# Kernel optimization log

Hardware: AMD Instinct MI355X
Metric: run time of the kernel (lower is better)

Reference implementation:

```python
import jax, jax.numpy as jnp
import numpy as np

N_POINTS = 100000
K_VOL = 27          # 3^3 hypercube kernel offsets
PAIRS = 60000       # active in/out pairs per kernel offset
C_IN = 64
C_OUT = 64


def setup_inputs() -> dict:
    key = jax.random.key(0)
    k1, k2, k3, k4, k5 = jax.random.split(key, 5)
    stdv = 1.0 / np.sqrt(C_IN * K_VOL)  # matches reset_parameters
    inputs = {
        "input": jax.random.normal(k1, (N_POINTS, C_IN), dtype=jnp.float32),
        "kernel": jax.random.uniform(k2, (K_VOL, C_IN, C_OUT), dtype=jnp.float32,
                                      minval=-stdv, maxval=stdv),
        "bias": jax.random.uniform(k3, (1, C_OUT), dtype=jnp.float32,
                                    minval=-stdv, maxval=stdv),
        # per-offset kernel maps (normally produced from coordinate hashing in metadata)
        "in_map": jax.random.randint(k4, (K_VOL, PAIRS), 0, N_POINTS, dtype=jnp.int32),
        "out_map": jax.random.randint(k5, (K_VOL, PAIRS), 0, N_POINTS, dtype=jnp.int32),
    }
    return inputs


def reference(input, kernel, bias, in_map, out_map):
    # Sparse convolution: for each kernel offset k, gather input rows via
    # in_map[k], apply the per-offset GEMM with kernel[k], and scatter-add
    # the results into the output rows given by out_map[k].
    K, P = in_map.shape
    n_out = input.shape[0]
    gathered = input[in_map]                         # [K, P, Cin]  (gather)
    per_offset = jnp.einsum('kpi,kio->kpo', gathered, kernel)  # [K, P, Cout] (GEMM)
    out = jax.ops.segment_sum(per_offset.reshape(K * P, -1),
                              out_map.reshape(-1),
                              num_segments=n_out)    # [N, Cout] (scatter-add)
    return out + bias
```

## Files before the change

### kernel.cpp

```cpp
#include <hip/hip_runtime.h>
#include <hip/hip_bf16.h>

#define N_POINTS 100000
#define K_VOL 27
#define PAIRS 60000
#define CCH 64
#define TILES_PER_K (PAIRS / 16)
#define BX 64
#define NWAVES 4

#define RPB 64
#define NBUCKETS ((N_POINTS + RPB - 1) / RPB)
#define NBINS (NBUCKETS * K_VOL)
#define CAP 96
#define SENT 0xFFFFFFFFu
#define CNTSTRIDE 32

#define PREP_BLKS 6250
#define FILL_BLKS (K_VOL * 64)
#define PSUB (PAIRS / 8)
#define NLB 200

#define WS_ENT 0
#define WS_CNT (NBINS * CAP * 4)
#define WS_INBF (WS_CNT + NBUCKETS * CNTSTRIDE * 4)
#define WS_WT (WS_INBF + N_POINTS * CCH * 2)
#define WS_NEED (WS_WT + K_VOL * CCH * CCH * 2)

typedef __bf16 bf16x8 __attribute__((ext_vector_type(8)));
typedef __bf16 bf16x4 __attribute__((ext_vector_type(4)));
typedef float f32x4 __attribute__((ext_vector_type(4)));


__global__ __launch_bounds__(256) void prep_fill_kernel(
    const float* __restrict__ input, const float* __restrict__ weight,
    const int* __restrict__ in_map, const int* __restrict__ out_map,
    unsigned char* __restrict__ ws) {
  const int bid = blockIdx.x;
  if (bid < PREP_BLKS) {
    int t = bid * 256 + threadIdx.x;
    float4 v = ((const float4*)input)[t];
    bf16x4 o;
    o[0] = (__bf16)v.x; o[1] = (__bf16)v.y; o[2] = (__bf16)v.z; o[3] = (__bf16)v.w;
    *(bf16x4*)(ws + WS_INBF + (size_t)t * 8) = o;
    if (t < K_VOL * CCH * CCH) {
      int k = t >> 12;
      int r = t & 4095;
      int ci = r >> 6, co = r & 63;
      *(__bf16*)(ws + WS_WT + (size_t)(((k * 64 + co) << 6) + ci) * 2) =
          (__bf16)weight[t];
    }
  } else {
    __shared__ unsigned int lcnt[NLB];
    __shared__ unsigned int lcur[NLB];
    const int f = bid - PREP_BLKS;
    const int k = f >> 6;
    const int bx = f & 63;
    const int slice = bx & 7;
    const int sub = bx >> 3;
    const int pbeg = sub * PSUB, pend = pbeg + PSUB;
    const int* omp_ = out_map + k * PAIRS;
    const int* imp_ = in_map + k * PAIRS;
    unsigned int* cntp = (unsigned int*)(ws + WS_CNT);
    unsigned int* entp = (unsigned int*)(ws + WS_ENT);

    for (int i = threadIdx.x; i < NLB; i += 256) lcnt[i] = 0;
    __syncthreads();

    for (int p = pbeg + (int)threadIdx.x * 4; p < pend; p += 1024) {
      int4 om4 = *(const int4*)(omp_ + p);
      int oms[4] = {om4.x, om4.y, om4.z, om4.w};
#pragma unroll
      for (int j = 0; j < 4; ++j) {
        int bkt = oms[j] >> 6;
        if ((bkt & 7) == slice) atomicAdd(&lcnt[bkt >> 3], 1u);
      }
    }
    __syncthreads();

    for (int lb = threadIdx.x; lb < NLB; lb += 256) {
      unsigned n = lcnt[lb];
      if (n) {
        int bkt = (lb << 3) | slice;
        lcur[lb] = atomicAdd(cntp + (bkt << 5) + k, n);
      }
    }
    __syncthreads();

    for (int p = pbeg + (int)threadIdx.x * 4; p < pend; p += 1024) {
      int4 om4 = *(const int4*)(omp_ + p);
      int4 im4 = *(const int4*)(imp_ + p);
      int oms[4] = {om4.x, om4.y, om4.z, om4.w};
      int ims[4] = {im4.x, im4.y, im4.z, im4.w};
#pragma unroll
      for (int j = 0; j < 4; ++j) {
        int bkt = oms[j] >> 6;
        if ((bkt & 7) != slice) continue;
        unsigned pos = atomicAdd(&lcur[bkt >> 3], 1u);
        if (pos < CAP)
          entp[(bkt * K_VOL + k) * CAP + pos] =
              (unsigned)ims[j] | ((unsigned)(oms[j] & 63) << 17);
      }
    }
  }
}

__global__ __launch_bounds__(256) void spconv_main_kernel(
    const float* __restrict__ bias, const unsigned char* __restrict__ ws,
    float* __restrict__ out) {
  __shared__ __align__(16) unsigned char lds[4 * 8192];
  const unsigned int* cnt = (const unsigned int*)(ws + WS_CNT);
  const unsigned int* entries = (const unsigned int*)(ws + WS_ENT);
  const __bf16* inbf = (const __bf16*)(ws + WS_INBF);
  const __bf16* wt = (const __bf16*)(ws + WS_WT);

  const int b = blockIdx.x;
  const int tid = threadIdx.x;
  const int wave = tid >> 6, lane = tid & 63;
  const int c = lane & 15, q = lane >> 4;
  unsigned char* stage = lds + wave * 8192;
  unsigned char* pmat = stage + 4096;

#pragma unroll
  for (int i = 0; i < 16; ++i)
    *(float*)(pmat + i * 256 + lane * 4) = 0.f;

  f32x4 acc[4][4];
#pragma unroll
  for (int rb = 0; rb < 4; ++rb)
#pragma unroll
    for (int nt = 0; nt < 4; ++nt) acc[rb][nt] = (f32x4){0.f, 0.f, 0.f, 0.f};

  bf16x8 bfA0[4], bfA1[4];

  auto grow = [&](unsigned v, bf16x8& x0, bf16x8& x1) {
    unsigned r = (v == SENT) ? 0u : (v & 0x1FFFFu);
    const __bf16* ar = inbf + ((size_t)r << 6);
    x0 = *(const bf16x8*)(ar + q * 8);
    x1 = *(const bf16x8*)(ar + 32 + q * 8);
  };

  auto do_tile = [&](unsigned entL, unsigned entH, bf16x8 aL0, bf16x8 aL1,
                     bf16x8 aH0, bf16x8 aH1) {
    int mol0 = -1, mol1 = -1;
    if (q == 0 && entL != SENT) mol0 = (int)(entL >> 17);
    if (q == 1 && entH != SENT) mol1 = (int)(entH >> 17);
    if (mol0 >= 0) {
      int m = c;
      *(__bf16*)(pmat + mol0 * 64 + (((m >> 3) ^ (mol0 & 3)) << 4) + (m & 7) * 2) =
          (__bf16)1.0f;
    }
    if (mol1 >= 0) {
      int m = 16 + c;
      *(__bf16*)(pmat + mol1 * 64 + (((m >> 3) ^ (mol1 & 3)) << 4) + (m & 7) * 2) =
          (__bf16)1.0f;
    }

    f32x4 c1a[4], c1b[4];
#pragma unroll
    for (int nt = 0; nt < 4; ++nt) {
      c1a[nt] = (f32x4){0.f, 0.f, 0.f, 0.f};
      c1b[nt] = (f32x4){0.f, 0.f, 0.f, 0.f};
    }
#pragma unroll
    for (int nt = 0; nt < 4; ++nt) {
      c1a[nt] = __builtin_amdgcn_mfma_f32_16x16x32_bf16(aL0, bfA0[nt], c1a[nt],
                                                        0, 0, 0);
      c1a[nt] = __builtin_amdgcn_mfma_f32_16x16x32_bf16(aL1, bfA1[nt], c1a[nt],
                                                        0, 0, 0);
      c1b[nt] = __builtin_amdgcn_mfma_f32_16x16x32_bf16(aH0, bfA0[nt], c1b[nt],
                                                        0, 0, 0);
      c1b[nt] = __builtin_amdgcn_mfma_f32_16x16x32_bf16(aH1, bfA1[nt], c1b[nt],
                                                        0, 0, 0);
    }

#pragma unroll
    for (int nt = 0; nt < 4; ++nt) {
      const int n = nt * 16 + c;
      const int swz = n & 3;
      const int in0 = (q & 1) * 8;
      bf16x4 h0, h1;
#pragma unroll
      for (int r = 0; r < 4; ++r) {
        h0[r] = (__bf16)c1a[nt][r];
        h1[r] = (__bf16)c1b[nt][r];
      }
      *(bf16x4*)(stage + n * 64 + (((q >> 1) ^ swz) << 4) + in0) = h0;
      *(bf16x4*)(stage + n * 64 + (((2 + (q >> 1)) ^ swz) << 4) + in0) = h1;
    }

    bf16x8 pfrag[4];
#pragma unroll
    for (int rb = 0; rb < 4; ++rb)
      pfrag[rb] = *(const bf16x8*)(pmat + (rb * 16 + c) * 64 + ((q ^ (c & 3)) << 4));
#pragma unroll
    for (int nt = 0; nt < 4; ++nt) {
      const int n = nt * 16 + c;
      const bf16x8 bb = *(const bf16x8*)(stage + n * 64 + ((q ^ (n & 3)) << 4));
#pragma unroll
      for (int rb = 0; rb < 4; ++rb)
        acc[rb][nt] = __builtin_amdgcn_mfma_f32_16x16x32_bf16(pfrag[rb], bb,
                                                             acc[rb][nt], 0, 0, 0);
    }

    if (mol0 >= 0) {
      int m = c;
      *(__bf16*)(pmat + mol0 * 64 + (((m >> 3) ^ (mol0 & 3)) << 4) + (m & 7) * 2) =
          (__bf16)0.0f;
    }
    if (mol1 >= 0) {
      int m = 16 + c;
      *(__bf16*)(pmat + mol1 * 64 + (((m >> 3) ^ (mol1 & 3)) << 4) + (m & 7) * 2) =
          (__bf16)0.0f;
    }
  };

  int j = wave;
  unsigned ec, w0, w1, w2, w3;
  bf16x8 qa00, qa01, qa10, qa11, qa20, qa21, qa30, qa31;
  unsigned ecn, x0, x1, x2, x3;
  {
    unsigned cn0 = cnt[(b << 5) + j];
    const unsigned* bp0 = entries + (size_t)(b * K_VOL + j) * CAP;
    unsigned a0 = bp0[c], a1 = bp0[16 + c], a2 = bp0[32 + c], a3 = bp0[48 + c];
    unsigned cn1 = 0, b0 = SENT, b1 = SENT, b2 = SENT, b3 = SENT;
    if (j + 4 < K_VOL) {
      cn1 = cnt[(b << 5) + j + 4];
      const unsigned* bp1 = entries + (size_t)(b * K_VOL + j + 4) * CAP;
      b0 = bp1[c]; b1 = bp1[16 + c]; b2 = bp1[32 + c]; b3 = bp1[48 + c];
    }
    ec = cn0 > CAP ? (unsigned)CAP : cn0;
    w0 = ((unsigned)c < ec) ? a0 : SENT;
    w1 = ((unsigned)(16 + c) < ec) ? a1 : SENT;
    w2 = ((unsigned)(32 + c) < ec) ? a2 : SENT;
    w3 = ((unsigned)(48 + c) < ec) ? a3 : SENT;
    grow(w0, qa00, qa01); grow(w1, qa10, qa11);
    grow(w2, qa20, qa21); grow(w3, qa30, qa31);
    ecn = cn1 > CAP ? (unsigned)CAP : cn1;
    x0 = ((unsigned)c < ecn) ? b0 : SENT;
    x1 = ((unsigned)(16 + c) < ecn) ? b1 : SENT;
    x2 = ((unsigned)(32 + c) < ecn) ? b2 : SENT;
    x3 = ((unsigned)(48 + c) < ecn) ? b3 : SENT;
  }
#pragma unroll
  for (int nt = 0; nt < 4; ++nt) {
    const __bf16* wrow = wt + ((j * 64 + nt * 16 + c) << 6);
    bfA0[nt] = *(const bf16x8*)(wrow + q * 8);
    bfA1[nt] = *(const bf16x8*)(wrow + 32 + q * 8);
  }

  while (j < K_VOL) {
    const int jn = j + 4, jf = j + 8;
    const bool hasn = jn < K_VOL, hasf = jf < K_VOL;

    bf16x8 pa00, pa01, pa10, pa11, pa20, pa21, pa30, pa31;
    if (hasn) {
      grow(x0, pa00, pa01); grow(x1, pa10, pa11);
      grow(x2, pa20, pa21); grow(x3, pa30, pa31);
    }

    unsigned fc = 0, h0 = SENT, h1 = SENT, h2 = SENT, h3 = SENT;
    if (hasf) {
      fc = cnt[(b << 5) + jf];
      const unsigned* bpf = entries + (size_t)(b * K_VOL + jf) * CAP;
      h0 = bpf[c]; h1 = bpf[16 + c]; h2 = bpf[32 + c]; h3 = bpf[48 + c];
    }

    if (ec) do_tile(w0, w1, qa00, qa01, qa10, qa11);
    if (ec > 32) do_tile(w2, w3, qa20, qa21, qa30, qa31);
    for (unsigned tb = 64; tb < ec; tb += 32) {
      const unsigned* base = entries + (size_t)(b * K_VOL + j) * CAP;
      unsigned i0 = tb + c, i1 = tb + 16 + c;
      unsigned e0 = (i0 < ec) ? base[i0] : SENT;
      unsigned e1 = (i1 < ec) ? base[i1] : SENT;
      bf16x8 y00, y01, y10, y11;
      grow(e0, y00, y01);
      grow(e1, y10, y11);
      do_tile(e0, e1, y00, y01, y10, y11);
    }

    if (hasn) {
#pragma unroll
      for (int nt = 0; nt < 4; ++nt) {
        const __bf16* wrow = wt + ((jn * 64 + nt * 16 + c) << 6);
        bfA0[nt] = *(const bf16x8*)(wrow + q * 8);
        bfA1[nt] = *(const bf16x8*)(wrow + 32 + q * 8);
      }
    }

    ec = ecn;
    w0 = x0; w1 = x1; w2 = x2; w3 = x3;
    qa00 = pa00; qa01 = pa01; qa10 = pa10; qa11 = pa11;
    qa20 = pa20; qa21 = pa21; qa30 = pa30; qa31 = pa31;
    ecn = fc > CAP ? (unsigned)CAP : fc;
    x0 = ((unsigned)c < ecn) ? h0 : SENT;
    x1 = ((unsigned)(16 + c) < ecn) ? h1 : SENT;
    x2 = ((unsigned)(32 + c) < ecn) ? h2 : SENT;
    x3 = ((unsigned)(48 + c) < ecn) ? h3 : SENT;
    j = jn;
  }

  __syncthreads();
  float* bufA = (float*)lds;
  float* bufB = (float*)(lds + 16384);

  auto REDST = [&](float* buf) {
#pragma unroll
    for (int rb = 0; rb < 4; ++rb)
#pragma unroll
      for (int nt = 0; nt < 4; ++nt)
#pragma unroll
        for (int r = 0; r < 4; ++r) {
          int row = rb * 16 + q * 4 + r;
          int col = (nt * 16 + c) ^ (q << 2) ^ ((q & 1) << 4);
          buf[row * 64 + col] = acc[rb][nt][r];
        }
  };
  auto REDADD = [&](const float* buf) {
#pragma unroll
    for (int rb = 0; rb < 4; ++rb)
#pragma unroll
      for (int nt = 0; nt < 4; ++nt)
#pragma unroll
        for (int r = 0; r < 4; ++r) {
          int row = rb * 16 + q * 4 + r;
          int col = (nt * 16 + c) ^ (q << 2) ^ ((q & 1) << 4);
          acc[rb][nt][r] += buf[row * 64 + col];
        }
  };

  if (wave == 1) REDST(bufA);
  if (wave == 3) REDST(bufB);
  __syncthreads();
  if (wave == 0) REDADD(bufA);
  if (wave == 2) REDADD(bufB);
  __syncthreads();
  if (wave == 2) REDST(bufA);
  __syncthreads();
  if (wave == 0) {
    REDADD(bufA);
    float bv[4];
#pragma unroll
    for (int nt = 0; nt < 4; ++nt) bv[nt] = bias[nt * 16 + c];
#pragma unroll
    for (int rb = 0; rb < 4; ++rb)
#pragma unroll
      for (int r = 0; r < 4; ++r) {
        const int row = b * RPB + rb * 16 + q * 4 + r;
        if (row < N_POINTS) {
#pragma unroll
          for (int nt = 0; nt < 4; ++nt)
            out[row * CCH + nt * 16 + c] = acc[rb][nt][r] + bv[nt];
        }
      }
  }
}


__global__ __launch_bounds__(256) void init_out_kernel(
    const float* __restrict__ bias, float* __restrict__ out) {
  int tid = blockIdx.x * blockDim.x + threadIdx.x;
  int c4 = tid & 15;
  float4 b = ((const float4*)bias)[c4];
  ((float4*)out)[tid] = b;
}

__global__ __launch_bounds__(256) void spconv_kernel(
    const float* __restrict__ input, const float* __restrict__ weight,
    const int* __restrict__ in_map, const int* __restrict__ out_map,
    float* __restrict__ out) {
  const int k = blockIdx.y;
  const int lane = threadIdx.x & 63;
  const int wave = threadIdx.x >> 6;
  const int col = lane & 15;
  const int quad = lane >> 4;

  const float* Wk = weight + k * (CCH * CCH);
  bf16x8 bfrag[4][2];
#pragma unroll
  for (int nt = 0; nt < 4; ++nt) {
    int co = nt * 16 + col;
#pragma unroll
    for (int s = 0; s < 2; ++s) {
      int ci0 = s * 32 + quad * 8;
      bf16x8 f;
#pragma unroll
      for (int j = 0; j < 8; ++j) f[j] = (__bf16)Wk[(ci0 + j) * CCH + co];
      bfrag[nt][s] = f;
    }
  }

  const int* im = in_map + k * PAIRS;
  const int* om = out_map + k * PAIRS;

  for (int tile = blockIdx.x * NWAVES + wave; tile < TILES_PER_K;
       tile += BX * NWAVES) {
    const int pbase = tile * 16;
    int rin = im[pbase + col];
    const float* arow = input + rin * CCH;
    bf16x8 afrag[2];
#pragma unroll
    for (int s = 0; s < 2; ++s) {
      const float4 x0 = *(const float4*)(arow + s * 32 + quad * 8);
      const float4 x1 = *(const float4*)(arow + s * 32 + quad * 8 + 4);
      bf16x8 f;
      f[0] = (__bf16)x0.x; f[1] = (__bf16)x0.y;
      f[2] = (__bf16)x0.z; f[3] = (__bf16)x0.w;
      f[4] = (__bf16)x1.x; f[5] = (__bf16)x1.y;
      f[6] = (__bf16)x1.z; f[7] = (__bf16)x1.w;
      afrag[s] = f;
    }

    f32x4 acc[4];
#pragma unroll
    for (int nt = 0; nt < 4; ++nt) acc[nt] = (f32x4){0.f, 0.f, 0.f, 0.f};
#pragma unroll
    for (int nt = 0; nt < 4; ++nt) {
      acc[nt] = __builtin_amdgcn_mfma_f32_16x16x32_bf16(afrag[0], bfrag[nt][0],
                                                        acc[nt], 0, 0, 0);
      acc[nt] = __builtin_amdgcn_mfma_f32_16x16x32_bf16(afrag[1], bfrag[nt][1],
                                                        acc[nt], 0, 0, 0);
    }

    int orow[4];
#pragma unroll
    for (int r = 0; r < 4; ++r) orow[r] = om[pbase + quad * 4 + r];
#pragma unroll
    for (int r = 0; r < 4; ++r) {
      float* op = out + orow[r] * CCH + col;
#pragma unroll
      for (int nt = 0; nt < 4; ++nt) atomicAdd(op + nt * 16, acc[nt][r]);
    }
  }
}


extern "C" void kernel_launch(void* const* d_in, const int* in_sizes, int n_in,
                              void* d_out, int out_size, void* d_ws,
                              size_t ws_size, hipStream_t stream) {
  const float* input = (const float*)d_in[0];
  const float* weight = (const float*)d_in[1];
  const float* bias = (const float*)d_in[2];
  const int* in_map = (const int*)d_in[3];
  const int* out_map = (const int*)d_in[4];
  float* out = (float*)d_out;

  if (d_ws != nullptr && ws_size >= (size_t)WS_NEED) {
    unsigned char* ws = (unsigned char*)d_ws;
    hipMemsetAsync(ws + WS_CNT, 0, NBUCKETS * CNTSTRIDE * 4, stream);
    prep_fill_kernel<<<PREP_BLKS + FILL_BLKS, 256, 0, stream>>>(
        input, weight, in_map, out_map, ws);
    spconv_main_kernel<<<NBUCKETS, 256, 0, stream>>>(bias, ws, out);
  } else {
    init_out_kernel<<<(N_POINTS * 16) / 256, 256, 0, stream>>>(bias, out);
    dim3 grid(BX, K_VOL);
    spconv_kernel<<<grid, 256, 0, stream>>>(input, weight, in_map, out_map, out);
  }
}
```

Baseline: 227.2 us.

## Buffer bucket entries in LDS during fill and change LDS swizzle pattern

The fill phase now reads in_map and out_map only once. It stages each pair's packed entry in a per-bucket LDS buffer, with an overflow path that appends directly to global memory via atomics. The buffered entries are then copied out per bucket after the global offset is reserved. This removes the second pass over the maps and the scattered global writes. Separately, the XOR swizzle for the pmat and stage LDS tiles now keys on (row>>1)&3 instead of row&3, to reduce LDS bank conflicts for the 8-byte and 16-byte accesses. The overflow path could reorder entries and adds atomic contention, and the larger shared buffer raises LDS use per fill block.

```diff
diff --git a/kernel.cpp b/kernel.cpp
--- a/kernel.cpp
+++ b/kernel.cpp
@@ -20,6 +20,7 @@
 #define FILL_BLKS (K_VOL * 64)
 #define PSUB (PAIRS / 8)
 #define NLB 200
+#define CAPL 24
 
 #define WS_ENT 0
 #define WS_CNT (NBINS * CAP * 4)
@@ -53,6 +54,7 @@
   } else {
     __shared__ unsigned int lcnt[NLB];
     __shared__ unsigned int lcur[NLB];
+    __shared__ unsigned int lbuf[NLB * CAPL];
     const int f = bid - PREP_BLKS;
     const int k = f >> 6;
     const int bx = f & 63;
@@ -69,11 +71,23 @@
 
     for (int p = pbeg + (int)threadIdx.x * 4; p < pend; p += 1024) {
       int4 om4 = *(const int4*)(omp_ + p);
+      int4 im4 = *(const int4*)(imp_ + p);
       int oms[4] = {om4.x, om4.y, om4.z, om4.w};
+      int ims[4] = {im4.x, im4.y, im4.z, im4.w};
 #pragma unroll
       for (int j = 0; j < 4; ++j) {
         int bkt = oms[j] >> 6;
-        if ((bkt & 7) == slice) atomicAdd(&lcnt[bkt >> 3], 1u);
+        if ((bkt & 7) != slice) continue;
+        int lb = bkt >> 3;
+        unsigned ent = (unsigned)ims[j] | ((unsigned)(oms[j] & 63) << 17);
+        unsigned pos = atomicAdd(&lcnt[lb], 1u);
+        if (pos < CAPL) {
+          lbuf[lb * CAPL + pos] = ent;
+        } else {
+          atomicSub(&lcnt[lb], 1u);
+          unsigned gp = atomicAdd(cntp + (bkt << 5) + k, 1u);
+          if (gp < CAP) entp[(size_t)(bkt * K_VOL + k) * CAP + gp] = ent;
+        }
       }
     }
     __syncthreads();
@@ -87,19 +101,15 @@
     }
     __syncthreads();
 
-    for (int p = pbeg + (int)threadIdx.x * 4; p < pend; p += 1024) {
-      int4 om4 = *(const int4*)(omp_ + p);
-      int4 im4 = *(const int4*)(imp_ + p);
-      int oms[4] = {om4.x, om4.y, om4.z, om4.w};
-      int ims[4] = {im4.x, im4.y, im4.z, im4.w};
-#pragma unroll
-      for (int j = 0; j < 4; ++j) {
-        int bkt = oms[j] >> 6;
-        if ((bkt & 7) != slice) continue;
-        unsigned pos = atomicAdd(&lcur[bkt >> 3], 1u);
-        if (pos < CAP)
-          entp[(bkt * K_VOL + k) * CAP + pos] =
-              (unsigned)ims[j] | ((unsigned)(oms[j] & 63) << 17);
+    for (int lb = threadIdx.x; lb < NLB; lb += 256) {
+      unsigned n = lcnt[lb];
+      if (!n) continue;
+      int bkt = (lb << 3) | slice;
+      unsigned base = lcur[lb];
+      unsigned int* dst = entp + (size_t)(bkt * K_VOL + k) * CAP;
+      for (unsigned i = 0; i < n; ++i) {
+        unsigned pos = base + i;
+        if (pos < CAP) dst[pos] = lbuf[lb * CAPL + i];
       }
     }
   }
@@ -147,13 +157,13 @@
     if (q == 1 && entH != SENT) mol1 = (int)(entH >> 17);
     if (mol0 >= 0) {
       int m = c;
-      *(__bf16*)(pmat + mol0 * 64 + (((m >> 3) ^ (mol0 & 3)) << 4) + (m & 7) * 2) =
-          (__bf16)1.0f;
+      *(__bf16*)(pmat + mol0 * 64 + (((m >> 3) ^ ((mol0 >> 1) & 3)) << 4) +
+                 (m & 7) * 2) = (__bf16)1.0f;
     }
     if (mol1 >= 0) {
       int m = 16 + c;
-      *(__bf16*)(pmat + mol1 * 64 + (((m >> 3) ^ (mol1 & 3)) << 4) + (m & 7) * 2) =
-          (__bf16)1.0f;
+      *(__bf16*)(pmat + mol1 * 64 + (((m >> 3) ^ ((mol1 >> 1) & 3)) << 4) +
+                 (m & 7) * 2) = (__bf16)1.0f;
     }
 
     f32x4 c1a[4], c1b[4];
@@ -177,7 +187,7 @@
 #pragma unroll
     for (int nt = 0; nt < 4; ++nt) {
       const int n = nt * 16 + c;
-      const int swz = n & 3;
+      const int swz = (n >> 1) & 3;
       const int in0 = (q & 1) * 8;
       bf16x4 h0, h1;
 #pragma unroll
@@ -192,11 +202,13 @@
     bf16x8 pfrag[4];
 #pragma unroll
     for (int rb = 0; rb < 4; ++rb)
-      pfrag[rb] = *(const bf16x8*)(pmat + (rb * 16 + c) * 64 + ((q ^ (c & 3)) << 4));
+      pfrag[rb] = *(const bf16x8*)(pmat + (rb * 16 + c) * 64 +
+                                   ((q ^ ((c >> 1) & 3)) << 4));
 #pragma unroll
     for (int nt = 0; nt < 4; ++nt) {
       const int n = nt * 16 + c;
-      const bf16x8 bb = *(const bf16x8*)(stage + n * 64 + ((q ^ (n & 3)) << 4));
+      const bf16x8 bb = *(const bf16x8*)(stage + n * 64 +
+                                         ((q ^ ((n >> 1) & 3)) << 4));
 #pragma unroll
       for (int rb = 0; rb < 4; ++rb)
         acc[rb][nt] = __builtin_amdgcn_mfma_f32_16x16x32_bf16(pfrag[rb], bb,
@@ -205,13 +217,13 @@
 
     if (mol0 >= 0) {
       int m = c;
-      *(__bf16*)(pmat + mol0 * 64 + (((m >> 3) ^ (mol0 & 3)) << 4) + (m & 7) * 2) =
-          (__bf16)0.0f;
+      *(__bf16*)(pmat + mol0 * 64 + (((m >> 3) ^ ((mol0 >> 1) & 3)) << 4) +
+                 (m & 7) * 2) = (__bf16)0.0f;
     }
     if (mol1 >= 0) {
       int m = 16 + c;
-      *(__bf16*)(pmat + mol1 * 64 + (((m >> 3) ^ (mol1 & 3)) << 4) + (m & 7) * 2) =
-          (__bf16)0.0f;
+      *(__bf16*)(pmat + mol1 * 64 + (((m >> 3) ^ ((mol1 >> 1) & 3)) << 4) +
+                 (m & 7) * 2) = (__bf16)0.0f;
     }
   };
 
```

Result: faster. 215.0 us (-5.4%).
